# Kernel optimization log

Measured on AMD Instinct MI355X. Metric: run time of the kernel, lower is better.

Reference implementation:

```python
import jax, jax.numpy as jnp
import numpy as np

B, S, D, H = 2, 2048, 2048, 16
DH = D // H  # 128
MAX_SEQ = 2048


def _rope_tables(dim, max_seq_len):
    inv_freq = 1.0 / (10000.0 ** (jnp.arange(0, dim, 2, dtype=jnp.float32) / dim))
    t = jnp.arange(max_seq_len, dtype=jnp.float32)
    freqs = jnp.einsum('i,j->ij', t, inv_freq)          # [S, dim/2]
    emb = jnp.concatenate([freqs, freqs], axis=-1)       # [S, dim]
    return jnp.cos(emb), jnp.sin(emb)


def setup_inputs() -> dict:
    key = jax.random.key(0)
    kx, kq, kk, kv, ko = jax.random.split(key, 5)
    scale = 1.0 / np.sqrt(D)
    x = jax.random.normal(kx, (B, S, D), dtype=jnp.float32)
    # nn.Linear weights: [out_features, in_features], y = x @ W.T
    wq = jax.random.normal(kq, (H * DH, D), dtype=jnp.float32) * scale
    wk = jax.random.normal(kk, (H * DH, D), dtype=jnp.float32) * scale
    wv = jax.random.normal(kv, (H * DH, D), dtype=jnp.float32) * scale
    wo = jax.random.normal(ko, (D, H * DH), dtype=jnp.float32) * scale
    cos, sin = _rope_tables(DH, MAX_SEQ)
    return {"x": x, "wq": wq, "wk": wk, "wv": wv, "wo": wo,
            "cos": cos, "sin": sin}


def _rotate(t):
    # faithful to torch: cat([-t[..., 1::2], t[..., ::2]], dim=-1)
    return jnp.concatenate([-t[..., 1::2], t[..., ::2]], axis=-1)


def reference(x, wq, wk, wv, wo, cos, sin):
    b, s, _ = x.shape
    # QKV projections -> [b, h, s, dh]
    def proj(w):
        return jnp.einsum('bsd,ed->bse', x, w).reshape(b, s, H, DH).transpose(0, 2, 1, 3)
    q, k, v = proj(wq), proj(wk), proj(wv)
    c = cos[:s, :]  # [s, dh], broadcasts over b, h
    si = sin[:s, :]
    q = q * c + _rotate(q) * si
    k = k * c + _rotate(k) * si
    # scaled dot-product attention, non-causal
    scores = jnp.einsum('bhqd,bhkd->bhqk', q, k) / np.sqrt(DH)
    attn = jax.nn.softmax(scores, axis=-1)
    out = jnp.einsum('bhqk,bhkd->bhqd', attn, v)
    out = out.transpose(0, 2, 1, 3).reshape(b, s, H * DH)
    return jnp.einsum('bse,de->bsd', out, wo)
```

## Files before the change

kernel.cpp:

```cpp
#include <hip/hip_runtime.h>

#define SQ   2048
#define DIMD 2048
#define NH   16
#define HD   128
#define MR   4096
#define QBLK 128
#define KBLK 64

using u16 = unsigned short;
using u32 = unsigned int;
using s16x8 = __attribute__((ext_vector_type(8))) short;
using u16x8 = __attribute__((ext_vector_type(8))) unsigned short;
using f32x4 = __attribute__((ext_vector_type(4))) float;
using as3u  = __attribute__((address_space(3))) u32;
using as1u  = __attribute__((address_space(1))) u32;

__device__ __forceinline__ u16 f2bf(float f) {
  u32 x = __float_as_uint(f);
  return (u16)((x + 0x7fffu + ((x >> 16) & 1u)) >> 16);
}
__device__ __forceinline__ float bf2f(u16 u) {
  return __uint_as_float(((u32)u) << 16);
}
__device__ __forceinline__ void gld16(const void* g, void* l) {
  __builtin_amdgcn_global_load_lds((as1u*)g, (as3u*)l, 16, 0, 0);
}

__global__ __launch_bounds__(256) void cvt_bf16(const float* __restrict__ s,
                                                u16* __restrict__ d, int n4) {
  int i = blockIdx.x * 256 + threadIdx.x;
  int st = gridDim.x * 256;
  for (; i < n4; i += st) {
    float4 v = ((const float4*)s)[i];
    u32 lo = (u32)f2bf(v.x) | ((u32)f2bf(v.y) << 16);
    u32 hi = (u32)f2bf(v.z) | ((u32)f2bf(v.w) << 16);
    ((uint2*)d)[i] = make_uint2(lo, hi);
  }
}

__global__ __launch_bounds__(256) void rope_kernel(
    const u16* __restrict__ Qin, const u16* __restrict__ Kin,
    u16* __restrict__ Qout, u16* __restrict__ Kout,
    const float* __restrict__ cosT, const float* __restrict__ sinT) {
  int ten = blockIdx.y;
  const u16* in = ten ? Kin : Qin;
  u16* outp     = ten ? Kout : Qout;
  float scl     = ten ? 1.0f : 0.08838834764831845f;
  int row = blockIdx.x * 4 + (threadIdx.x >> 6);
  int j   = threadIdx.x & 63;
  int s   = row & (SQ - 1);
  const u16* r = in + (size_t)row * HD;
  u16* w = outp + (size_t)row * HD;
  float c  = cosT[s * HD + j];
  float si = sinT[s * HD + j];
  float a  = bf2f(r[j]);
  float b  = bf2f(r[j + 64]);
  float ev = bf2f(r[2 * j]);
  float od = bf2f(r[2 * j + 1]);
  w[j]      = f2bf((a * c - od * si) * scl);
  w[j + 64] = f2bf((b * c + ev * si) * scl);
}

__global__ __launch_bounds__(256) void transpose_v(const u16* __restrict__ V,
                                                   u16* __restrict__ Vt) {
  __shared__ u16 tile[64][72];
  int sb = blockIdx.x, db = blockIdx.y, bh = blockIdx.z;
  int r  = threadIdx.x >> 3;
  int c8 = (threadIdx.x & 7) * 8;
  const u16* src = V + ((size_t)bh * SQ + sb * 64) * HD + db * 64;
#pragma unroll
  for (int p2 = 0; p2 < 2; p2++) {
    int row = p2 * 32 + r;
    u16x8 v = *(const u16x8*)(src + (size_t)row * HD + c8);
#pragma unroll
    for (int k2 = 0; k2 < 8; k2++) tile[row][c8 + k2] = v[k2];
  }
  __syncthreads();
  u16* dst = Vt + ((size_t)bh * HD + db * 64) * SQ + sb * 64;
#pragma unroll
  for (int p2 = 0; p2 < 2; p2++) {
    int dr = p2 * 32 + r;
    u16x8 o;
#pragma unroll
    for (int k2 = 0; k2 < 8; k2++) o[k2] = tile[c8 + k2][dr];
    *(u16x8*)(dst + (size_t)dr * SQ + c8) = o;
  }
}

template <int MODE>
__global__ __launch_bounds__(256) void gemm_bt(
    const u16* __restrict__ A,
    const u16* __restrict__ W0, const u16* __restrict__ W1, const u16* __restrict__ W2,
    u16* __restrict__ O0, u16* __restrict__ O1, u16* __restrict__ O2,
    float* __restrict__ Ofp) {
  __shared__ alignas(16) u16 lA[2][128 * 32];
  __shared__ alignas(16) u16 lB[2][128 * 32];
  int t = threadIdx.x;
  int l = t & 63, l15 = l & 15, lg = l >> 4;
  int wid = t >> 6, wr = wid >> 1, wc = wid & 1;
  int mi = blockIdx.x >> 4, ni = blockIdx.x & 15;
  int m0 = mi * 128, n0 = ni * 128;
  const u16* W = W0;
  u16* Ob = O0;
  if (MODE == 0) {
    if (blockIdx.y == 1) { W = W1; Ob = O1; }
    else if (blockIdx.y == 2) { W = W2; Ob = O2; }
  }
  const u16* Ag = A + (size_t)m0 * DIMD;
  const u16* Wg = W + (size_t)n0 * DIMD;
  int r0 = t >> 2, ch = (t & 3) * 8;

  f32x4 acc[4][4];
#pragma unroll
  for (int a1 = 0; a1 < 4; a1++)
#pragma unroll
    for (int b1 = 0; b1 < 4; b1++) acc[a1][b1] = (f32x4){0.f, 0.f, 0.f, 0.f};

  auto stage = [&](int buf, int kb) {
    int k0 = kb * 32;
    gld16(Ag + (size_t)r0 * DIMD + k0 + ch,        &lA[buf][t * 8]);
    gld16(Ag + (size_t)(r0 + 64) * DIMD + k0 + ch, &lA[buf][(t + 256) * 8]);
    gld16(Wg + (size_t)r0 * DIMD + k0 + ch,        &lB[buf][t * 8]);
    gld16(Wg + (size_t)(r0 + 64) * DIMD + k0 + ch, &lB[buf][(t + 256) * 8]);
  };

  stage(0, 0);
  __syncthreads();
#pragma unroll 2
  for (int kb = 0; kb < DIMD / 32; kb++) {
    if (kb + 1 < DIMD / 32) stage((kb + 1) & 1, kb + 1);
    int buf = kb & 1;
    s16x8 af[4], bfr[4];
#pragma unroll
    for (int rb = 0; rb < 4; rb++)
      af[rb] = *(const s16x8*)&lA[buf][(wr * 64 + rb * 16 + l15) * 32 + lg * 8];
#pragma unroll
    for (int cb = 0; cb < 4; cb++)
      bfr[cb] = *(const s16x8*)&lB[buf][(wc * 64 + cb * 16 + l15) * 32 + lg * 8];
#pragma unroll
    for (int rb = 0; rb < 4; rb++)
#pragma unroll
      for (int cb = 0; cb < 4; cb++)
        acc[rb][cb] = __builtin_amdgcn_mfma_f32_16x16x32_bf16(af[rb], bfr[cb], acc[rb][cb], 0, 0, 0);
    __syncthreads();
  }
#pragma unroll
  for (int rb = 0; rb < 4; rb++) {
#pragma unroll
    for (int cb = 0; cb < 4; cb++) {
#pragma unroll
      for (int i = 0; i < 4; i++) {
        float v = acc[rb][cb][i];
        int mm = m0 + wr * 64 + rb * 16 + lg * 4 + i;
        int nn = n0 + wc * 64 + cb * 16 + l15;
        if (MODE == 0) {
          int b = mm >> 11, s2 = mm & (SQ - 1), h = nn >> 7, dh = nn & (HD - 1);
          Ob[((size_t)(b * NH + h) * SQ + s2) * HD + dh] = f2bf(v);
        } else {
          Ofp[(size_t)mm * DIMD + nn] = v;
        }
      }
    }
  }
}

__global__ __launch_bounds__(512, 4) void attn_kernel(
    const u16* __restrict__ Q, const u16* __restrict__ K,
    const u16* __restrict__ Vt, u16* __restrict__ Aout) {
  __shared__ alignas(16) u16 Ksh[2][KBLK * HD];
  __shared__ alignas(16) u16 Vsh[2][HD * KBLK];
  __shared__ alignas(16) u16 Pl[8][16 * KBLK];
  int t = threadIdx.x;
  int wid = t >> 6, l = t & 63, l15 = l & 15, lg = l >> 4;
  int orig = blockIdx.x;
  int bid = (orig & 7) * 64 + (orig >> 3);
  int qb = bid & 15, bh = bid >> 4;
  int q0 = qb * QBLK + wid * 16;
  const u16* Qb = Q + ((size_t)bh * SQ + q0) * HD;
  const u16* Kb = K + (size_t)bh * SQ * HD;
  const u16* Vb = Vt + (size_t)bh * HD * SQ;

  s16x8 qf[4];
#pragma unroll
  for (int ks = 0; ks < 4; ks++)
    qf[ks] = *(const s16x8*)(Qb + (size_t)l15 * HD + ks * 32 + lg * 8);

  int o0 = t * 16, o1 = t * 16 + 8192;
  int kr0 = o0 >> 8, kc0 = (o0 & 255) ^ ((kr0 & 7) << 4);
  int kr1 = o1 >> 8, kc1 = (o1 & 255) ^ ((kr1 & 7) << 4);
  int vr0 = o0 >> 7, vc0 = (o0 & 127) ^ ((vr0 & 7) << 4);
  int vr1 = o1 >> 7, vc1 = (o1 & 127) ^ ((vr1 & 7) << 4);

  auto stage = [&](int buf, int kb) {
    const u16* Kt = Kb + (size_t)kb * KBLK * HD;
    const u16* Vs = Vb + kb * KBLK;
    gld16(Kt + (size_t)kr0 * HD + (kc0 >> 1), &Ksh[buf][o0 >> 1]);
    gld16(Kt + (size_t)kr1 * HD + (kc1 >> 1), &Ksh[buf][o1 >> 1]);
    gld16(Vs + (size_t)vr0 * SQ + (vc0 >> 1), &Vsh[buf][o0 >> 1]);
    gld16(Vs + (size_t)vr1 * SQ + (vc1 >> 1), &Vsh[buf][o1 >> 1]);
  };

  f32x4 acc[8];
#pragma unroll
  for (int i = 0; i < 8; i++) acc[i] = (f32x4){0.f, 0.f, 0.f, 0.f};
  float m = -3.0e38f, lsum = 0.f;

  stage(0, 0);
  __syncthreads();

#pragma unroll 1
  for (int kb = 0; kb < SQ / KBLK; kb++) {
    int cur = kb & 1;
    if (kb + 1 < SQ / KBLK) stage(cur ^ 1, kb + 1);
    f32x4 sa[4];
#pragma unroll
    for (int cb = 0; cb < 4; cb++) sa[cb] = (f32x4){0.f, 0.f, 0.f, 0.f};
    __builtin_amdgcn_s_setprio(1);
#pragma unroll
    for (int ks = 0; ks < 4; ks++) {
#pragma unroll
      for (int cb = 0; cb < 4; cb++) {
        int r = cb * 16 + l15;
        int off = r * 256 + ((ks * 64 + lg * 16) ^ ((r & 7) << 4));
        s16x8 kf = *(const s16x8*)((const char*)&Ksh[cur][0] + off);
        sa[cb] = __builtin_amdgcn_mfma_f32_16x16x32_bf16(kf, qf[ks], sa[cb], 0, 0, 0);
      }
    }
    __builtin_amdgcn_s_setprio(0);
    float rm = sa[0][0];
#pragma unroll
    for (int cb = 0; cb < 4; cb++)
#pragma unroll
      for (int i = 0; i < 4; i++) rm = fmaxf(rm, sa[cb][i]);
    rm = fmaxf(rm, __shfl_xor(rm, 16));
    rm = fmaxf(rm, __shfl_xor(rm, 32));
    if (!__all(rm <= m + 8.0f)) {
      float mn = fmaxf(m, rm);
      float al = __expf(m - mn);
      m = mn;
      float alq[4];
#pragma unroll
      for (int i = 0; i < 4; i++) alq[i] = __shfl(al, lg * 4 + i, 16);
#pragma unroll
      for (int c2 = 0; c2 < 8; c2++)
#pragma unroll
        for (int i = 0; i < 4; i++) acc[c2][i] *= alq[i];
      lsum *= al;
    }
    float ps = 0.f;
#pragma unroll
    for (int cb = 0; cb < 4; cb++)
#pragma unroll
      for (int i = 0; i < 4; i++) {
        sa[cb][i] = __expf(sa[cb][i] - m);
        ps += sa[cb][i];
      }
    ps += __shfl_xor(ps, 16);
    ps += __shfl_xor(ps, 32);
    lsum += ps;
#pragma unroll
    for (int cb = 0; cb < 4; cb++) {
      u32 lo = (u32)f2bf(sa[cb][0]) | ((u32)f2bf(sa[cb][1]) << 16);
      u32 hi = (u32)f2bf(sa[cb][2]) | ((u32)f2bf(sa[cb][3]) << 16);
      int off = l15 * 128 + ((cb * 32 + lg * 8) ^ ((l15 & 7) << 4));
      *(uint2*)((char*)&Pl[wid][0] + off) = make_uint2(lo, hi);
    }
    asm volatile("s_waitcnt lgkmcnt(0)" ::: "memory");
    __builtin_amdgcn_sched_barrier(0);
    s16x8 pf[2];
#pragma unroll
    for (int k2 = 0; k2 < 2; k2++) {
      int off = l15 * 128 + ((k2 * 64 + lg * 16) ^ ((l15 & 7) << 4));
      pf[k2] = *(const s16x8*)((const char*)&Pl[wid][0] + off);
    }
    __builtin_amdgcn_s_setprio(1);
#pragma unroll
    for (int c2 = 0; c2 < 8; c2++) {
#pragma unroll
      for (int k2 = 0; k2 < 2; k2++) {
        int r = c2 * 16 + l15;
        int off = r * 128 + ((k2 * 64 + lg * 16) ^ ((r & 7) << 4));
        s16x8 vf = *(const s16x8*)((const char*)&Vsh[cur][0] + off);
        acc[c2] = __builtin_amdgcn_mfma_f32_16x16x32_bf16(pf[k2], vf, acc[c2], 0, 0, 0);
      }
    }
    __builtin_amdgcn_s_setprio(0);
    __syncthreads();
  }
  float rin = 1.0f / lsum;
  float rq[4];
#pragma unroll
  for (int i = 0; i < 4; i++) rq[i] = __shfl(rin, lg * 4 + i, 16);
  int b = bh >> 4, h = bh & (NH - 1);
#pragma unroll
  for (int c2 = 0; c2 < 8; c2++) {
#pragma unroll
    for (int i = 0; i < 4; i++) {
      int q = q0 + lg * 4 + i;
      int dh = c2 * 16 + l15;
      Aout[((size_t)b * SQ + q) * DIMD + h * HD + dh] = f2bf(acc[c2][i] * rq[i]);
    }
  }
}

extern "C" void kernel_launch(void* const* d_in, const int* in_sizes, int n_in,
                              void* d_out, int out_size, void* d_ws, size_t ws_size,
                              hipStream_t stream) {
  (void)in_sizes; (void)n_in; (void)out_size; (void)ws_size;
  const float* x    = (const float*)d_in[0];
  const float* wq   = (const float*)d_in[1];
  const float* wk   = (const float*)d_in[2];
  const float* wv   = (const float*)d_in[3];
  const float* wo   = (const float*)d_in[4];
  const float* cosT = (const float*)d_in[5];
  const float* sinT = (const float*)d_in[6];
  float* out = (float*)d_out;

  char* p = (char*)d_ws;
  const size_t SZ_MD = (size_t)MR * DIMD * 2;
  const size_t SZ_W  = (size_t)DIMD * DIMD * 2;
  u16* xb   = (u16*)p; p += SZ_MD;
  u16* wqb  = (u16*)p; p += SZ_W;
  u16* wkb  = (u16*)p; p += SZ_W;
  u16* wvb  = (u16*)p; p += SZ_W;
  u16* wob  = (u16*)p; p += SZ_W;
  u16* Qraw = (u16*)p; p += SZ_MD;
  u16* Kraw = (u16*)p; p += SZ_MD;
  u16* Qr   = (u16*)p; p += SZ_MD;
  u16* Kr   = (u16*)p; p += SZ_MD;
  u16* Vb   = (u16*)p; p += SZ_MD;
  u16* Vt   = (u16*)p; p += SZ_MD;
  u16* attnout = Qraw;

  cvt_bf16<<<1024, 256, 0, stream>>>(x,  xb,  MR * DIMD / 4);
  cvt_bf16<<<512,  256, 0, stream>>>(wq, wqb, DIMD * DIMD / 4);
  cvt_bf16<<<512,  256, 0, stream>>>(wk, wkb, DIMD * DIMD / 4);
  cvt_bf16<<<512,  256, 0, stream>>>(wv, wvb, DIMD * DIMD / 4);
  cvt_bf16<<<512,  256, 0, stream>>>(wo, wob, DIMD * DIMD / 4);

  gemm_bt<0><<<dim3(512, 3), 256, 0, stream>>>(xb, wqb, wkb, wvb, Qraw, Kraw, Vb, nullptr);
  rope_kernel<<<dim3(16384, 2), 256, 0, stream>>>(Qraw, Kraw, Qr, Kr, cosT, sinT);
  transpose_v<<<dim3(32, 2, 32), 256, 0, stream>>>(Vb, Vt);
  attn_kernel<<<512, 512, 0, stream>>>(Qr, Kr, Vt, attnout);
  gemm_bt<1><<<dim3(512, 1), 256, 0, stream>>>(attnout, wob, nullptr, nullptr,
                                               nullptr, nullptr, nullptr, out);
}
```

Baseline: 334.2 us.

## Replace projection GEMMs with 8-wave 128x256 ping-pong pipelined kernel

```diff
diff --git a/kernel.cpp b/kernel.cpp
--- a/kernel.cpp
+++ b/kernel.cpp
@@ -26,6 +26,7 @@
 __device__ __forceinline__ void gld16(const void* g, void* l) {
   __builtin_amdgcn_global_load_lds((as1u*)g, (as3u*)l, 16, 0, 0);
 }
+#define MFMA16 __builtin_amdgcn_mfma_f32_16x16x32_bf16
 
 __global__ __launch_bounds__(256) void cvt_bf16(const float* __restrict__ s,
                                                 u16* __restrict__ d, int n4) {
@@ -89,27 +90,21 @@
 }
 
 template <int MODE>
-__global__ __launch_bounds__(256) void gemm_bt(
-    const u16* __restrict__ A,
-    const u16* __restrict__ W0, const u16* __restrict__ W1, const u16* __restrict__ W2,
-    u16* __restrict__ O0, u16* __restrict__ O1, u16* __restrict__ O2,
-    float* __restrict__ Ofp) {
-  __shared__ alignas(16) u16 lA[2][128 * 32];
-  __shared__ alignas(16) u16 lB[2][128 * 32];
+__global__ __launch_bounds__(512, 2) void gemm8p(
+    const u16* __restrict__ A, const u16* __restrict__ W,
+    u16* __restrict__ Obf, float* __restrict__ Ofp) {
+  __shared__ alignas(16) u16 lA[2][2][128 * 32];
+  __shared__ alignas(16) u16 lB[2][2][256 * 32];
   int t = threadIdx.x;
   int l = t & 63, l15 = l & 15, lg = l >> 4;
-  int wid = t >> 6, wr = wid >> 1, wc = wid & 1;
-  int mi = blockIdx.x >> 4, ni = blockIdx.x & 15;
-  int m0 = mi * 128, n0 = ni * 128;
-  const u16* W = W0;
-  u16* Ob = O0;
-  if (MODE == 0) {
-    if (blockIdx.y == 1) { W = W1; Ob = O1; }
-    else if (blockIdx.y == 2) { W = W2; Ob = O2; }
-  }
+  int wid = t >> 6, wm = wid >> 2, wn = wid & 3;
+  int orig = blockIdx.x;
+  int NBX = (MODE == 0) ? 96 : 32;
+  int li = (orig & 7) * NBX + (orig >> 3);
+  int mB = li & 31, nB = li >> 5;
+  int m0 = mB * 128, n0 = nB * 256;
   const u16* Ag = A + (size_t)m0 * DIMD;
   const u16* Wg = W + (size_t)n0 * DIMD;
-  int r0 = t >> 2, ch = (t & 3) * 8;
 
   f32x4 acc[4][4];
 #pragma unroll
@@ -117,46 +112,126 @@
 #pragma unroll
     for (int b1 = 0; b1 < 4; b1++) acc[a1][b1] = (f32x4){0.f, 0.f, 0.f, 0.f};
 
-  auto stage = [&](int buf, int kb) {
-    int k0 = kb * 32;
-    gld16(Ag + (size_t)r0 * DIMD + k0 + ch,        &lA[buf][t * 8]);
-    gld16(Ag + (size_t)(r0 + 64) * DIMD + k0 + ch, &lA[buf][(t + 256) * 8]);
-    gld16(Wg + (size_t)r0 * DIMD + k0 + ch,        &lB[buf][t * 8]);
-    gld16(Wg + (size_t)(r0 + 64) * DIMD + k0 + ch, &lB[buf][(t + 256) * 8]);
+  int bo0 = t * 16, bo1 = t * 16 + 8192;
+  int br0 = bo0 >> 6, bc0 = (bo0 & 63) >> 1;
+  int br1 = bo1 >> 6, bc1 = (bo1 & 63) >> 1;
+
+  auto stageB = [&](int buf, int kt, int kh) {
+    const u16* src = Wg + kt * 64 + kh * 32;
+    gld16(src + (size_t)br0 * DIMD + bc0, &lB[buf][kh][bo0 >> 1]);
+    gld16(src + (size_t)br1 * DIMD + bc1, &lB[buf][kh][bo1 >> 1]);
   };
-
-  stage(0, 0);
-  __syncthreads();
-#pragma unroll 2
-  for (int kb = 0; kb < DIMD / 32; kb++) {
-    if (kb + 1 < DIMD / 32) stage((kb + 1) & 1, kb + 1);
-    int buf = kb & 1;
-    s16x8 af[4], bfr[4];
-#pragma unroll
-    for (int rb = 0; rb < 4; rb++)
-      af[rb] = *(const s16x8*)&lA[buf][(wr * 64 + rb * 16 + l15) * 32 + lg * 8];
-#pragma unroll
-    for (int cb = 0; cb < 4; cb++)
-      bfr[cb] = *(const s16x8*)&lB[buf][(wc * 64 + cb * 16 + l15) * 32 + lg * 8];
-#pragma unroll
-    for (int rb = 0; rb < 4; rb++)
-#pragma unroll
-      for (int cb = 0; cb < 4; cb++)
-        acc[rb][cb] = __builtin_amdgcn_mfma_f32_16x16x32_bf16(af[rb], bfr[cb], acc[rb][cb], 0, 0, 0);
-    __syncthreads();
-  }
-#pragma unroll
-  for (int rb = 0; rb < 4; rb++) {
-#pragma unroll
-    for (int cb = 0; cb < 4; cb++) {
+  auto stageA = [&](int buf, int kt, int kh) {
+    const u16* src = Ag + kt * 64 + kh * 32;
+    gld16(src + (size_t)br0 * DIMD + bc0, &lA[buf][kh][bo0 >> 1]);
+  };
+  auto rdA = [&](int buf, int kh, int mf) {
+    return *(const s16x8*)&lA[buf][kh][(wm * 64 + mf * 16 + l15) * 32 + lg * 8];
+  };
+  auto rdB = [&](int buf, int kh, int nf) {
+    return *(const s16x8*)&lB[buf][kh][(wn * 64 + nf * 16 + l15) * 32 + lg * 8];
+  };
+
+  const int NKT = DIMD / 64;
+  stageB(0, 0, 0);
+  stageA(0, 0, 0);
+  stageB(0, 0, 1);
+  stageA(0, 0, 1);
+  asm volatile("s_waitcnt vmcnt(3)" ::: "memory");
+  __builtin_amdgcn_s_barrier();
+
+#pragma unroll 1
+  for (int kt = 0; kt < NKT; kt++) {
+    int buf = kt & 1, nbuf = buf ^ 1;
+    int ktn = (kt + 1 < NKT) ? kt + 1 : kt;
+    s16x8 bf0, bf1, bf2, bf3, af0, af1;
+    bf0 = rdB(buf, 0, 0); bf1 = rdB(buf, 0, 1);
+    bf2 = rdB(buf, 0, 2); bf3 = rdB(buf, 0, 3);
+    af0 = rdA(buf, 0, 0); af1 = rdA(buf, 0, 1);
+    stageB(nbuf, ktn, 0);
+    __builtin_amdgcn_s_barrier();
+    asm volatile("s_waitcnt lgkmcnt(0)" ::: "memory");
+    __builtin_amdgcn_sched_barrier(0);
+    __builtin_amdgcn_s_setprio(1);
+    acc[0][0] = MFMA16(af0, bf0, acc[0][0], 0, 0, 0);
+    acc[0][1] = MFMA16(af0, bf1, acc[0][1], 0, 0, 0);
+    acc[0][2] = MFMA16(af0, bf2, acc[0][2], 0, 0, 0);
+    acc[0][3] = MFMA16(af0, bf3, acc[0][3], 0, 0, 0);
+    acc[1][0] = MFMA16(af1, bf0, acc[1][0], 0, 0, 0);
+    acc[1][1] = MFMA16(af1, bf1, acc[1][1], 0, 0, 0);
+    acc[1][2] = MFMA16(af1, bf2, acc[1][2], 0, 0, 0);
+    acc[1][3] = MFMA16(af1, bf3, acc[1][3], 0, 0, 0);
+    __builtin_amdgcn_s_setprio(0);
+    __builtin_amdgcn_s_barrier();
+    af0 = rdA(buf, 0, 2); af1 = rdA(buf, 0, 3);
+    stageA(nbuf, ktn, 0);
+    __builtin_amdgcn_s_barrier();
+    asm volatile("s_waitcnt lgkmcnt(0)" ::: "memory");
+    __builtin_amdgcn_sched_barrier(0);
+    __builtin_amdgcn_s_setprio(1);
+    acc[2][0] = MFMA16(af0, bf0, acc[2][0], 0, 0, 0);
+    acc[2][1] = MFMA16(af0, bf1, acc[2][1], 0, 0, 0);
+    acc[2][2] = MFMA16(af0, bf2, acc[2][2], 0, 0, 0);
+    acc[2][3] = MFMA16(af0, bf3, acc[2][3], 0, 0, 0);
+    acc[3][0] = MFMA16(af1, bf0, acc[3][0], 0, 0, 0);
+    acc[3][1] = MFMA16(af1, bf1, acc[3][1], 0, 0, 0);
+    acc[3][2] = MFMA16(af1, bf2, acc[3][2], 0, 0, 0);
+    acc[3][3] = MFMA16(af1, bf3, acc[3][3], 0, 0, 0);
+    __builtin_amdgcn_s_setprio(0);
+    asm volatile("s_waitcnt vmcnt(3)" ::: "memory");
+    __builtin_amdgcn_s_barrier();
+    bf0 = rdB(buf, 1, 0); bf1 = rdB(buf, 1, 1);
+    bf2 = rdB(buf, 1, 2); bf3 = rdB(buf, 1, 3);
+    af0 = rdA(buf, 1, 0); af1 = rdA(buf, 1, 1);
+    stageB(nbuf, ktn, 1);
+    __builtin_amdgcn_s_barrier();
+    asm volatile("s_waitcnt lgkmcnt(0)" ::: "memory");
+    __builtin_amdgcn_sched_barrier(0);
+    __builtin_amdgcn_s_setprio(1);
+    acc[0][0] = MFMA16(af0, bf0, acc[0][0], 0, 0, 0);
+    acc[0][1] = MFMA16(af0, bf1, acc[0][1], 0, 0, 0);
+    acc[0][2] = MFMA16(af0, bf2, acc[0][2], 0, 0, 0);
+    acc[0][3] = MFMA16(af0, bf3, acc[0][3], 0, 0, 0);
+    acc[1][0] = MFMA16(af1, bf0, acc[1][0], 0, 0, 0);
+    acc[1][1] = MFMA16(af1, bf1, acc[1][1], 0, 0, 0);
+    acc[1][2] = MFMA16(af1, bf2, acc[1][2], 0, 0, 0);
+    acc[1][3] = MFMA16(af1, bf3, acc[1][3], 0, 0, 0);
+    __builtin_amdgcn_s_setprio(0);
+    __builtin_amdgcn_s_barrier();
+    af0 = rdA(buf, 1, 2); af1 = rdA(buf, 1, 3);
+    stageA(nbuf, ktn, 1);
+    __builtin_amdgcn_s_barrier();
+    asm volatile("s_waitcnt lgkmcnt(0)" ::: "memory");
+    __builtin_amdgcn_sched_barrier(0);
+    __builtin_amdgcn_s_setprio(1);
+    acc[2][0] = MFMA16(af0, bf0, acc[2][0], 0, 0, 0);
+    acc[2][1] = MFMA16(af0, bf1, acc[2][1], 0, 0, 0);
+    acc[2][2] = MFMA16(af0, bf2, acc[2][2], 0, 0, 0);
+    acc[2][3] = MFMA16(af0, bf3, acc[2][3], 0, 0, 0);
+    acc[3][0] = MFMA16(af1, bf0, acc[3][0], 0, 0, 0);
+    acc[3][1] = MFMA16(af1, bf1, acc[3][1], 0, 0, 0);
+    acc[3][2] = MFMA16(af1, bf2, acc[3][2], 0, 0, 0);
+    acc[3][3] = MFMA16(af1, bf3, acc[3][3], 0, 0, 0);
+    __builtin_amdgcn_s_setprio(0);
+    asm volatile("s_waitcnt vmcnt(3)" ::: "memory");
+    __builtin_amdgcn_s_barrier();
+  }
+
+#pragma unroll
+  for (int mf = 0; mf < 4; mf++) {
+#pragma unroll
+    for (int nf = 0; nf < 4; nf++) {
 #pragma unroll
       for (int i = 0; i < 4; i++) {
-        float v = acc[rb][cb][i];
-        int mm = m0 + wr * 64 + rb * 16 + lg * 4 + i;
-        int nn = n0 + wc * 64 + cb * 16 + l15;
+        float v = acc[mf][nf][i];
+        int mm = m0 + wm * 64 + mf * 16 + lg * 4 + i;
+        int nn = n0 + wn * 64 + nf * 16 + l15;
         if (MODE == 0) {
-          int b = mm >> 11, s2 = mm & (SQ - 1), h = nn >> 7, dh = nn & (HD - 1);
-          Ob[((size_t)(b * NH + h) * SQ + s2) * HD + dh] = f2bf(v);
+          int wsel = nn >> 11, n2 = nn & 2047;
+          int h = n2 >> 7, dh = n2 & (HD - 1);
+          int b = mm >> 11, s2 = mm & (SQ - 1);
+          Obf[(size_t)wsel * MR * HD * NH +
+              ((size_t)(b * NH + h) * SQ + s2) * HD + dh] = f2bf(v);
         } else {
           Ofp[(size_t)mm * DIMD + nn] = v;
         }
@@ -224,7 +299,7 @@
         int r = cb * 16 + l15;
         int off = r * 256 + ((ks * 64 + lg * 16) ^ ((r & 7) << 4));
         s16x8 kf = *(const s16x8*)((const char*)&Ksh[cur][0] + off);
-        sa[cb] = __builtin_amdgcn_mfma_f32_16x16x32_bf16(kf, qf[ks], sa[cb], 0, 0, 0);
+        sa[cb] = MFMA16(kf, qf[ks], sa[cb], 0, 0, 0);
       }
     }
     __builtin_amdgcn_s_setprio(0);
@@ -282,7 +357,7 @@
         int r = c2 * 16 + l15;
         int off = r * 128 + ((k2 * 64 + lg * 16) ^ ((r & 7) << 4));
         s16x8 vf = *(const s16x8*)((const char*)&Vsh[cur][0] + off);
-        acc[c2] = __builtin_amdgcn_mfma_f32_16x16x32_bf16(pf[k2], vf, acc[c2], 0, 0, 0);
+        acc[c2] = MFMA16(pf[k2], vf, acc[c2], 0, 0, 0);
       }
     }
     __builtin_amdgcn_s_setprio(0);
@@ -327,9 +402,9 @@
   u16* wob  = (u16*)p; p += SZ_W;
   u16* Qraw = (u16*)p; p += SZ_MD;
   u16* Kraw = (u16*)p; p += SZ_MD;
+  u16* Vraw = (u16*)p; p += SZ_MD;
   u16* Qr   = (u16*)p; p += SZ_MD;
   u16* Kr   = (u16*)p; p += SZ_MD;
-  u16* Vb   = (u16*)p; p += SZ_MD;
   u16* Vt   = (u16*)p; p += SZ_MD;
   u16* attnout = Qraw;
 
@@ -339,10 +414,9 @@
   cvt_bf16<<<512,  256, 0, stream>>>(wv, wvb, DIMD * DIMD / 4);
   cvt_bf16<<<512,  256, 0, stream>>>(wo, wob, DIMD * DIMD / 4);
 
-  gemm_bt<0><<<dim3(512, 3), 256, 0, stream>>>(xb, wqb, wkb, wvb, Qraw, Kraw, Vb, nullptr);
+  gemm8p<0><<<768, 512, 0, stream>>>(xb, wqb, Qraw, nullptr);
   rope_kernel<<<dim3(16384, 2), 256, 0, stream>>>(Qraw, Kraw, Qr, Kr, cosT, sinT);
-  transpose_v<<<dim3(32, 2, 32), 256, 0, stream>>>(Vb, Vt);
+  transpose_v<<<dim3(32, 2, 32), 256, 0, stream>>>(Vraw, Vt);
   attn_kernel<<<512, 512, 0, stream>>>(Qr, Kr, Vt, attnout);
-  gemm_bt<1><<<dim3(512, 1), 256, 0, stream>>>(attnout, wob, nullptr, nullptr,
-                                               nullptr, nullptr, nullptr, out);
-}
+  gemm8p<1><<<256, 512, 0, stream>>>(attnout, wob, nullptr, out);
+}
```

New measurement: 346.0 us. +3.6%, slower.

## Rewrite projection GEMMs with larger tiles, triple buffering and fused QKV

Applied to the files above, without the earlier changes.

```diff
diff --git a/kernel.cpp b/kernel.cpp
--- a/kernel.cpp
+++ b/kernel.cpp
@@ -26,6 +26,7 @@
 __device__ __forceinline__ void gld16(const void* g, void* l) {
   __builtin_amdgcn_global_load_lds((as1u*)g, (as3u*)l, 16, 0, 0);
 }
+#define MFMA16 __builtin_amdgcn_mfma_f32_16x16x32_bf16
 
 __global__ __launch_bounds__(256) void cvt_bf16(const float* __restrict__ s,
                                                 u16* __restrict__ d, int n4) {
@@ -89,74 +90,105 @@
 }
 
 template <int MODE>
-__global__ __launch_bounds__(256) void gemm_bt(
-    const u16* __restrict__ A,
-    const u16* __restrict__ W0, const u16* __restrict__ W1, const u16* __restrict__ W2,
-    u16* __restrict__ O0, u16* __restrict__ O1, u16* __restrict__ O2,
-    float* __restrict__ Ofp) {
-  __shared__ alignas(16) u16 lA[2][128 * 32];
-  __shared__ alignas(16) u16 lB[2][128 * 32];
+__global__ __launch_bounds__(512, 2) void gemm_tb(
+    const u16* __restrict__ A, const u16* __restrict__ W,
+    u16* __restrict__ Obf, float* __restrict__ Ofp) {
+  constexpr int BM  = (MODE == 0) ? 256 : 128;
+  constexpr int MF  = BM / 32;
+  constexpr int ALD = BM / 128;
+  __shared__ alignas(16) u16 lA[3][BM * 32];
+  __shared__ alignas(16) u16 lB[3][256 * 32];
   int t = threadIdx.x;
   int l = t & 63, l15 = l & 15, lg = l >> 4;
-  int wid = t >> 6, wr = wid >> 1, wc = wid & 1;
-  int mi = blockIdx.x >> 4, ni = blockIdx.x & 15;
-  int m0 = mi * 128, n0 = ni * 128;
-  const u16* W = W0;
-  u16* Ob = O0;
-  if (MODE == 0) {
-    if (blockIdx.y == 1) { W = W1; Ob = O1; }
-    else if (blockIdx.y == 2) { W = W2; Ob = O2; }
-  }
+  int wid = t >> 6, wm = wid >> 2, wn = wid & 3;
+  int orig = blockIdx.x;
+  constexpr int CPX = (MODE == 0) ? 48 : 32;
+  int li = (orig & 7) * CPX + (orig >> 3);
+  constexpr int MT = (MODE == 0) ? 16 : 32;
+  int mB = li % MT, nB = li / MT;
+  int m0 = mB * BM, n0 = nB * 256;
   const u16* Ag = A + (size_t)m0 * DIMD;
   const u16* Wg = W + (size_t)n0 * DIMD;
-  int r0 = t >> 2, ch = (t & 3) * 8;
-
-  f32x4 acc[4][4];
-#pragma unroll
-  for (int a1 = 0; a1 < 4; a1++)
+
+  f32x4 acc[MF][4];
+#pragma unroll
+  for (int a1 = 0; a1 < MF; a1++)
 #pragma unroll
     for (int b1 = 0; b1 < 4; b1++) acc[a1][b1] = (f32x4){0.f, 0.f, 0.f, 0.f};
 
-  auto stage = [&](int buf, int kb) {
-    int k0 = kb * 32;
-    gld16(Ag + (size_t)r0 * DIMD + k0 + ch,        &lA[buf][t * 8]);
-    gld16(Ag + (size_t)(r0 + 64) * DIMD + k0 + ch, &lA[buf][(t + 256) * 8]);
-    gld16(Wg + (size_t)r0 * DIMD + k0 + ch,        &lB[buf][t * 8]);
-    gld16(Wg + (size_t)(r0 + 64) * DIMD + k0 + ch, &lB[buf][(t + 256) * 8]);
+  int o0 = t * 16, o1 = t * 16 + 8192;
+  int br0 = o0 >> 6, ac0 = (o0 & 63) >> 1;
+  int br1 = o1 >> 6, ac1 = (o1 & 63) >> 1;
+
+  auto stage = [&](int buf, int kt) {
+    const u16* Ws = Wg + kt * 32;
+    const u16* As = Ag + kt * 32;
+    gld16(Ws + (size_t)br0 * DIMD + ac0, &lB[buf][o0 >> 1]);
+    gld16(Ws + (size_t)br1 * DIMD + ac1, &lB[buf][o1 >> 1]);
+    gld16(As + (size_t)br0 * DIMD + ac0, &lA[buf][o0 >> 1]);
+    if (ALD == 2) gld16(As + (size_t)br1 * DIMD + ac1, &lA[buf][o1 >> 1]);
   };
 
+  int aoff[MF], boff[4];
+#pragma unroll
+  for (int mf = 0; mf < MF; mf++) {
+    int r = wm * (BM / 2) + mf * 16 + l15;
+    aoff[mf] = r * 64 + lg * 16;
+  }
+#pragma unroll
+  for (int nf = 0; nf < 4; nf++) {
+    int r = wn * 64 + nf * 16 + l15;
+    boff[nf] = r * 64 + lg * 16;
+  }
+
+  const int NKT = DIMD / 32;
   stage(0, 0);
-  __syncthreads();
-#pragma unroll 2
-  for (int kb = 0; kb < DIMD / 32; kb++) {
-    if (kb + 1 < DIMD / 32) stage((kb + 1) & 1, kb + 1);
-    int buf = kb & 1;
-    s16x8 af[4], bfr[4];
-#pragma unroll
-    for (int rb = 0; rb < 4; rb++)
-      af[rb] = *(const s16x8*)&lA[buf][(wr * 64 + rb * 16 + l15) * 32 + lg * 8];
-#pragma unroll
-    for (int cb = 0; cb < 4; cb++)
-      bfr[cb] = *(const s16x8*)&lB[buf][(wc * 64 + cb * 16 + l15) * 32 + lg * 8];
-#pragma unroll
-    for (int rb = 0; rb < 4; rb++)
-#pragma unroll
-      for (int cb = 0; cb < 4; cb++)
-        acc[rb][cb] = __builtin_amdgcn_mfma_f32_16x16x32_bf16(af[rb], bfr[cb], acc[rb][cb], 0, 0, 0);
-    __syncthreads();
-  }
-#pragma unroll
-  for (int rb = 0; rb < 4; rb++) {
-#pragma unroll
-    for (int cb = 0; cb < 4; cb++) {
+  stage(1, 1);
+  if constexpr (MODE == 0) asm volatile("s_waitcnt vmcnt(4)" ::: "memory");
+  else                     asm volatile("s_waitcnt vmcnt(3)" ::: "memory");
+  __builtin_amdgcn_s_barrier();
+
+  int bcur = 0;
+#pragma unroll 1
+  for (int kt = 0; kt < NKT; kt++) {
+    int bnext = bcur + 2; if (bnext > 2) bnext -= 3;
+    int ksrc = kt + 2 < NKT ? kt + 2 : NKT - 1;
+    stage(bnext, ksrc);
+    const char* pa = (const char*)&lA[bcur][0];
+    const char* pb = (const char*)&lB[bcur][0];
+    s16x8 af[MF], bfr[4];
+#pragma unroll
+    for (int nf = 0; nf < 4; nf++) bfr[nf] = *(const s16x8*)(pb + boff[nf]);
+#pragma unroll
+    for (int mf = 0; mf < MF; mf++) af[mf] = *(const s16x8*)(pa + aoff[mf]);
+    __builtin_amdgcn_s_setprio(1);
+#pragma unroll
+    for (int mf = 0; mf < MF; mf++)
+#pragma unroll
+      for (int nf = 0; nf < 4; nf++)
+        acc[mf][nf] = MFMA16(af[mf], bfr[nf], acc[mf][nf], 0, 0, 0);
+    __builtin_amdgcn_s_setprio(0);
+    if constexpr (MODE == 0) asm volatile("s_waitcnt vmcnt(4)" ::: "memory");
+    else                     asm volatile("s_waitcnt vmcnt(3)" ::: "memory");
+    __builtin_amdgcn_s_barrier();
+    bcur = bcur + 1; if (bcur > 2) bcur -= 3;
+  }
+
+#pragma unroll
+  for (int mf = 0; mf < MF; mf++) {
+#pragma unroll
+    for (int nf = 0; nf < 4; nf++) {
 #pragma unroll
       for (int i = 0; i < 4; i++) {
-        float v = acc[rb][cb][i];
-        int mm = m0 + wr * 64 + rb * 16 + lg * 4 + i;
-        int nn = n0 + wc * 64 + cb * 16 + l15;
+        float v = acc[mf][nf][i];
+        int mm = m0 + wm * (BM / 2) + mf * 16 + lg * 4 + i;
+        int nn = n0 + wn * 64 + nf * 16 + l15;
         if (MODE == 0) {
-          int b = mm >> 11, s2 = mm & (SQ - 1), h = nn >> 7, dh = nn & (HD - 1);
-          Ob[((size_t)(b * NH + h) * SQ + s2) * HD + dh] = f2bf(v);
+          int wsel = nn >> 11, n2 = nn & 2047;
+          int h = n2 >> 7, dh = n2 & (HD - 1);
+          int b = mm >> 11, s2 = mm & (SQ - 1);
+          Obf[(size_t)wsel * MR * HD * NH +
+              ((size_t)(b * NH + h) * SQ + s2) * HD + dh] = f2bf(v);
         } else {
           Ofp[(size_t)mm * DIMD + nn] = v;
         }
@@ -224,7 +256,7 @@
         int r = cb * 16 + l15;
         int off = r * 256 + ((ks * 64 + lg * 16) ^ ((r & 7) << 4));
         s16x8 kf = *(const s16x8*)((const char*)&Ksh[cur][0] + off);
-        sa[cb] = __builtin_amdgcn_mfma_f32_16x16x32_bf16(kf, qf[ks], sa[cb], 0, 0, 0);
+        sa[cb] = MFMA16(kf, qf[ks], sa[cb], 0, 0, 0);
       }
     }
     __builtin_amdgcn_s_setprio(0);
@@ -282,7 +314,7 @@
         int r = c2 * 16 + l15;
         int off = r * 128 + ((k2 * 64 + lg * 16) ^ ((r & 7) << 4));
         s16x8 vf = *(const s16x8*)((const char*)&Vsh[cur][0] + off);
-        acc[c2] = __builtin_amdgcn_mfma_f32_16x16x32_bf16(pf[k2], vf, acc[c2], 0, 0, 0);
+        acc[c2] = MFMA16(pf[k2], vf, acc[c2], 0, 0, 0);
       }
     }
     __builtin_amdgcn_s_setprio(0);
@@ -327,9 +359,9 @@
   u16* wob  = (u16*)p; p += SZ_W;
   u16* Qraw = (u16*)p; p += SZ_MD;
   u16* Kraw = (u16*)p; p += SZ_MD;
+  u16* Vraw = (u16*)p; p += SZ_MD;
   u16* Qr   = (u16*)p; p += SZ_MD;
   u16* Kr   = (u16*)p; p += SZ_MD;
-  u16* Vb   = (u16*)p; p += SZ_MD;
   u16* Vt   = (u16*)p; p += SZ_MD;
   u16* attnout = Qraw;
 
@@ -339,10 +371,9 @@
   cvt_bf16<<<512,  256, 0, stream>>>(wv, wvb, DIMD * DIMD / 4);
   cvt_bf16<<<512,  256, 0, stream>>>(wo, wob, DIMD * DIMD / 4);
 
-  gemm_bt<0><<<dim3(512, 3), 256, 0, stream>>>(xb, wqb, wkb, wvb, Qraw, Kraw, Vb, nullptr);
+  gemm_tb<0><<<384, 512, 0, stream>>>(xb, wqb, Qraw, nullptr);
   rope_kernel<<<dim3(16384, 2), 256, 0, stream>>>(Qraw, Kraw, Qr, Kr, cosT, sinT);
-  transpose_v<<<dim3(32, 2, 32), 256, 0, stream>>>(Vb, Vt);
+  transpose_v<<<dim3(32, 2, 32), 256, 0, stream>>>(Vraw, Vt);
   attn_kernel<<<512, 512, 0, stream>>>(Qr, Kr, Vt, attnout);
-  gemm_bt<1><<<dim3(512, 1), 256, 0, stream>>>(attnout, wob, nullptr, nullptr,
-                                               nullptr, nullptr, nullptr, out);
-}
+  gemm_tb<1><<<256, 512, 0, stream>>>(attnout, wob, nullptr, out);
+}
```

Result: slower. 391.4 us (+17.1%).
